# Kernel tuning notes

Measured on AMD Instinct MI355X. Metric: run time of the kernel, lower is better.

## Reference

```python
import jax, jax.numpy as jnp
import numpy as np

N, H, NIN, A, P = 256, 1024, 512, 8, 2   # agents, hid_size, num_inputs, dim_actions, comm_passes
E = N * (N - 1)                          # directed complete graph (itertools.permutations order)
_src = np.repeat(np.arange(N), N - 1)
_dst = np.concatenate([np.concatenate([np.arange(i), np.arange(i + 1, N)]) for i in range(N)])


def setup_inputs() -> dict:
    key = jax.random.key(0)
    ks = jax.random.split(key, 30)
    rn = lambda k, sh, s=0.05: (jax.random.normal(k, sh, dtype=jnp.float32) * s)
    u = jax.random.uniform(ks[0], (P, 2, E, 2), jnp.float32, 1e-6, 1.0 - 1e-6)
    gumbel = -jnp.log(-jnp.log(u))
    inp = dict(
        x=jax.random.normal(ks[1], (N, NIN), jnp.float32),
        gumbel=gumbel,
        W_enc=rn(ks[2], (NIN, H)), b_enc=jnp.zeros((H,), jnp.float32),
        ha1_W1=rn(ks[3], (2 * H, H // 2)), ha1_b1=jnp.zeros((H // 2,), jnp.float32),
        ha1_W2=rn(ks[4], (H // 2, 2)), ha1_b2=jnp.zeros((2,), jnp.float32),
        ha2_W1=rn(ks[5], (2 * H, H // 2)), ha2_b1=jnp.zeros((H // 2,), jnp.float32),
        ha2_W2=rn(ks[6], (H // 2, 2)), ha2_b2=jnp.zeros((2,), jnp.float32),
        g1_W=rn(ks[7], (H, H)), g1_b=jnp.zeros((H,), jnp.float32),
        g2_W=rn(ks[8], (H, H)), g2_b=jnp.zeros((H,), jnp.float32),
        Wf=rn(ks[9], (P, H, H)), bf=jnp.zeros((P, H), jnp.float32),
        Wc=rn(ks[10], (P, H, H)), bc=jnp.zeros((P, H), jnp.float32),
        Wv=rn(ks[11], (H, 1)), bv=jnp.zeros((1,), jnp.float32),
        Wa=rn(ks[12], (H, A)), ba=jnp.zeros((A,), jnp.float32),
        log_std=jnp.zeros((1, A), jnp.float32),
    )
    return inp


def _edge_weights(h, W1, b1, W2, b2, g, src, dst):
    # concat(h[src], h[dst]) @ W1 == h[src] @ W1[:H] + h[dst] @ W1[H:]  (avoids [E,2H] concat)
    ps = h @ W1[:H]
    pd = h @ W1[H:]
    hid = jax.nn.relu(ps[src] + pd[dst] + b1)        # [E, H/2]
    logits = hid @ W2 + b2                            # [E, 2]
    y_soft = jax.nn.softmax(logits + g, axis=-1)      # gumbel-softmax, tau=1
    y_hard = jax.nn.one_hot(jnp.argmax(y_soft, axis=-1), 2, dtype=y_soft.dtype)
    y = y_hard + y_soft - jax.lax.stop_gradient(y_soft)  # straight-through hard
    return y[:, 1]                                    # edge selected iff class 1


def _gcn(h, w, Wg, bg, src, dst):
    # PyG GCNConv(normalize=False, add_self_loops=True): out_t = sum_{s->t} Wx_s + Wx_t + b
    Wx = h @ Wg                                       # [N, H]
    Adj = jnp.zeros((N, N), h.dtype).at[dst, src].set(w)  # Adj[t, s] = edge weight s->t
    return Adj @ Wx + Wx + bg


def reference(x, gumbel, W_enc, b_enc, ha1_W1, ha1_b1, ha1_W2, ha1_b2,
              ha2_W1, ha2_b1, ha2_W2, ha2_b2, g1_W, g1_b, g2_W, g2_b,
              Wf, bf, Wc, bc, Wv, bv, Wa, ba, log_std):
    src = jnp.asarray(_src)
    dst = jnp.asarray(_dst)
    x_enc = jnp.tanh(x @ W_enc + b_enc)               # non-recurrent encoder
    hidden = x_enc
    mask = jnp.ones((N, 1), x.dtype)                  # all agents alive
    for i in range(P):
        comm = hidden * mask
        w1 = _edge_weights(hidden, ha1_W1, ha1_b1, ha1_W2, ha1_b2, gumbel[i, 0], src, dst)
        comm = _gcn(comm, w1, g1_W, g1_b, src, dst)
        w2 = _edge_weights(comm, ha2_W1, ha2_b1, ha2_W2, ha2_b2, gumbel[i, 1], src, dst)
        comm = _gcn(comm, w2, g2_W, g2_b, src, dst)
        comm = comm * mask
        c = comm @ Wc[i] + bc[i]
        hidden = jnp.tanh(x_enc + (hidden @ Wf[i] + bf[i]) + c)
    value = hidden @ Wv + bv                          # [N, 1]
    h3 = hidden.reshape(1, N, H)
    a_mean = h3 @ Wa + ba                             # [1, N, A]
    a_log_std = jnp.broadcast_to(log_std, a_mean.shape)
    return a_mean, a_log_std, jnp.exp(a_log_std), value
```

## Files before the change

### kernel.cpp

```cpp
#include <hip/hip_runtime.h>

#define N_AG 256
#define HDIM 1024
#define NINP 512
#define EDG  65280

__device__ __forceinline__ int swz8(int b, int nw) {
  return (b & 7) * (nw >> 3) + (b >> 3);
}

__device__ __forceinline__ void gcore8(const float* __restrict__ Ap, const float* __restrict__ Bp,
                                       int kIters, int ldb, float acc[8]) {
  #pragma unroll 8
  for (int k=0; k<kIters; ++k) {
    float av = Ap[(size_t)k*N_AG];
    float4 b0 = *reinterpret_cast<const float4*>(Bp + (size_t)k*ldb);
    float4 b1 = *reinterpret_cast<const float4*>(Bp + (size_t)k*ldb + 4);
    acc[0]=fmaf(av,b0.x,acc[0]); acc[1]=fmaf(av,b0.y,acc[1]);
    acc[2]=fmaf(av,b0.z,acc[2]); acc[3]=fmaf(av,b0.w,acc[3]);
    acc[4]=fmaf(av,b1.x,acc[4]); acc[5]=fmaf(av,b1.y,acc[5]);
    acc[6]=fmaf(av,b1.z,acc[6]); acc[7]=fmaf(av,b1.w,acc[7]);
  }
}

__device__ __forceinline__ float kred8(const float acc[8], int lane, int wv, int tid) {
  __shared__ float red[8][64][9];
  #pragma unroll
  for (int j=0;j<8;++j) red[wv][lane][j] = acc[j];
  __syncthreads();
  int m = tid & 63, j = tid >> 6;
  float v = 0.f;
  #pragma unroll
  for (int w=0;w<8;++w) v += red[w][m][j];
  return v;
}

__global__ __launch_bounds__(512) void prep_k(const float* w2a, const float* b2a,
                                              const float* w2b, const float* b2b,
                                              float* wd1, float* wd2, float* bd) {
  int z = blockIdx.x;
  const float* W2 = z ? w2b : w2a;
  float* wd = z ? wd2 : wd1;
  int t = threadIdx.x;
  if (t < 512) wd[t] = W2[2*t+1] - W2[2*t];
  if (t == 0) { const float* b2 = z ? b2b : b2a; bd[z] = b2[1] - b2[0]; }
}

__global__ __launch_bounds__(256) void transpose_k(const float* __restrict__ x, float* __restrict__ xT) {
  __shared__ float tile[32][33];
  int tx = threadIdx.x, ty = threadIdx.y;
  int k0 = blockIdx.x*32, m0 = blockIdx.y*32;
  #pragma unroll
  for (int i=0;i<4;++i) tile[ty*4+i][tx] = x[(size_t)(m0+ty*4+i)*NINP + k0+tx];
  __syncthreads();
  #pragma unroll
  for (int i=0;i<4;++i) xT[(size_t)(k0+ty*4+i)*N_AG + m0+tx] = tile[tx][ty*4+i];
}

__global__ __launch_bounds__(512) void enc_k(const float* __restrict__ xT, const float* __restrict__ W,
                                             const float* __restrict__ b, float* __restrict__ xeT,
                                             float* __restrict__ hA) {
  int tid = threadIdx.x, lane = tid & 63;
  int wv = __builtin_amdgcn_readfirstlane(tid >> 6);
  int id = swz8(blockIdx.x, 512);
  int mb = id & 3, n0 = (id >> 2) * 8;
  int m  = mb*64 + lane;
  float acc[8] = {0,0,0,0,0,0,0,0};
  gcore8(xT + (size_t)(wv*64)*N_AG + m, W + (size_t)(wv*64)*HDIM + n0, 64, HDIM, acc);
  float v = kred8(acc, lane, wv, tid);
  int mo = mb*64 + (tid & 63);
  int n  = n0 + (tid >> 6);
  float t0 = tanhf(v + b[n]);
  xeT[(size_t)n*N_AG + mo] = t0;
  hA [(size_t)n*N_AG + mo] = t0;
}

__global__ __launch_bounds__(512) void fused_k(const float* __restrict__ hT,
    const float* __restrict__ W1a, const float* __restrict__ W1b, const float* __restrict__ b1,
    const float* __restrict__ gW, float* __restrict__ psT, float* __restrict__ pdT,
    float* __restrict__ Wx) {
  int tid = threadIdx.x, lane = tid & 63;
  int wv = __builtin_amdgcn_readfirstlane(tid >> 6);
  int id = swz8(blockIdx.x, 1024);
  int mb = id & 3, by = id >> 2;
  const float* B; int ldb, n0, mode;
  if (by < 64)       { B = W1a; ldb = 512;  n0 = by*8;       mode = 0; }
  else if (by < 128) { B = W1b; ldb = 512;  n0 = (by-64)*8;  mode = 1; }
  else               { B = gW;  ldb = HDIM; n0 = (by-128)*8; mode = 2; }
  int m = mb*64 + lane;
  float acc[8] = {0,0,0,0,0,0,0,0};
  gcore8(hT + (size_t)(wv*128)*N_AG + m, B + (size_t)(wv*128)*ldb + n0, 128, ldb, acc);
  float v = kred8(acc, lane, wv, tid);
  int mo = mb*64 + (tid & 63);
  int n  = n0 + (tid >> 6);
  if (mode == 0)      psT[(size_t)n*N_AG + mo] = v + b1[n];
  else if (mode == 1) pdT[(size_t)n*N_AG + mo] = v;
  else                Wx [(size_t)mo*HDIM + n] = v;
}

__global__ __launch_bounds__(256) void edge2_k(const float* __restrict__ psT,
    const float* __restrict__ pdT, const float* __restrict__ wd,
    const float* __restrict__ bdp, const float* __restrict__ g, float* __restrict__ AdjT) {
  __shared__ float red[4][65];
  int tid = threadIdx.x, lane = tid & 63;
  int wv = __builtin_amdgcn_readfirstlane(tid >> 6);
  int d  = blockIdx.x*64 + lane;
  int s  = blockIdx.y;
  const float* __restrict__ ps = psT + (size_t)(wv*128)*N_AG + s;
  const float* __restrict__ wp = wd + wv*128;
  const float* __restrict__ pp = pdT + (size_t)(wv*128)*N_AG + d;
  float acc = 0.f;
  #pragma unroll 8
  for (int k=0;k<128;++k)
    acc = fmaf(fmaxf(ps[(size_t)k*N_AG] + pp[(size_t)k*N_AG], 0.f), wp[k], acc);
  red[wv][lane] = acc;
  __syncthreads();
  if (wv == 0) {
    float tot = red[0][lane] + red[1][lane] + red[2][lane] + red[3][lane];
    int e = (d==s) ? 0 : (s*255 + d - (d>s ? 1 : 0));
    float g0 = g[2*e], g1 = g[2*e+1];
    float val = (tot + bdp[0] + g1 - g0) > 0.f ? 1.f : 0.f;
    if (d==s) val = 1.f;
    AdjT[(size_t)s*N_AG + d] = val;
  }
}

__global__ __launch_bounds__(512) void adj_k(const float* __restrict__ AdjT, const float* __restrict__ Wx,
                                             const float* __restrict__ gb, float* __restrict__ commT) {
  int tid = threadIdx.x, lane = tid & 63;
  int wv = __builtin_amdgcn_readfirstlane(tid >> 6);
  int id = swz8(blockIdx.x, 512);
  int mb = id & 3, n0 = (id >> 2) * 8;
  int m  = mb*64 + lane;
  float acc[8] = {0,0,0,0,0,0,0,0};
  gcore8(AdjT + (size_t)(wv*32)*N_AG + m, Wx + (size_t)(wv*32)*HDIM + n0, 32, HDIM, acc);
  float v = kred8(acc, lane, wv, tid);
  int mo = mb*64 + (tid & 63);
  int n  = n0 + (tid >> 6);
  commT[(size_t)n*N_AG + mo] = v + gb[n];
}

__global__ __launch_bounds__(512) void combine2_k(const float* __restrict__ hT, const float* __restrict__ cT,
    const float* __restrict__ Wf, const float* __restrict__ Wc, const float* __restrict__ xeT,
    const float* __restrict__ bfp, const float* __restrict__ bcp, float* __restrict__ hOut) {
  int tid = threadIdx.x, lane = tid & 63;
  int wv = __builtin_amdgcn_readfirstlane(tid >> 6);
  int id = swz8(blockIdx.x, 512);
  int mb = id & 3, n0 = (id >> 2) * 8;
  int m  = mb*64 + lane;
  int sel = wv >> 2, kb = (wv & 3)*256;
  const float* A = (sel ? cT : hT) + (size_t)kb*N_AG + m;
  const float* B = (sel ? Wc : Wf) + (size_t)kb*HDIM + n0;
  float acc[8] = {0,0,0,0,0,0,0,0};
  gcore8(A, B, 256, HDIM, acc);
  float v = kred8(acc, lane, wv, tid);
  int mo = mb*64 + (tid & 63);
  int n  = n0 + (tid >> 6);
  float r = v + xeT[(size_t)n*N_AG + mo] + bfp[n] + bcp[n];
  hOut[(size_t)n*N_AG + mo] = tanhf(r);
}

__global__ __launch_bounds__(256) void outinit_k(float* out, const float* ba, const float* ls, const float* bvp) {
  int t = blockIdx.x*256 + threadIdx.x;
  if (t < 2048) out[t] = ba[t & 7];
  else if (t < 4096) out[t] = ls[t & 7];
  else if (t < 6144) out[t] = expf(ls[t & 7]);
  else if (t < 6400) out[t] = bvp[0];
}

__global__ __launch_bounds__(64) void outpart_k(const float* __restrict__ hT, const float* __restrict__ Wa,
                                                const float* __restrict__ Wv, float* out) {
  int m = blockIdx.x*64 + threadIdx.x;
  int c0 = blockIdx.y*64;
  float acc[8] = {0,0,0,0,0,0,0,0};
  float av = 0.f;
  for (int c=c0; c<c0+64; ++c) {
    float h = hT[(size_t)c*N_AG + m];
    const float* wa = Wa + (size_t)c*8;
    #pragma unroll
    for (int j=0;j<8;++j) acc[j] = fmaf(h, wa[j], acc[j]);
    av = fmaf(h, Wv[c], av);
  }
  #pragma unroll
  for (int j=0;j<8;++j) atomicAdd(&out[m*8+j], acc[j]);
  atomicAdd(&out[6144+m], av);
}

extern "C" void kernel_launch(void* const* d_in, const int* in_sizes, int n_in,
                              void* d_out, int out_size, void* d_ws, size_t ws_size,
                              hipStream_t stream) {
  const float* x     = (const float*)d_in[0];
  const float* gum   = (const float*)d_in[1];
  const float* W_enc = (const float*)d_in[2];
  const float* b_enc = (const float*)d_in[3];
  const float* ha1W1 = (const float*)d_in[4];
  const float* ha1b1 = (const float*)d_in[5];
  const float* ha1W2 = (const float*)d_in[6];
  const float* ha1b2 = (const float*)d_in[7];
  const float* ha2W1 = (const float*)d_in[8];
  const float* ha2b1 = (const float*)d_in[9];
  const float* ha2W2 = (const float*)d_in[10];
  const float* ha2b2 = (const float*)d_in[11];
  const float* g1W = (const float*)d_in[12];
  const float* g1b = (const float*)d_in[13];
  const float* g2W = (const float*)d_in[14];
  const float* g2b = (const float*)d_in[15];
  const float* Wf  = (const float*)d_in[16];
  const float* bfp = (const float*)d_in[17];
  const float* Wc  = (const float*)d_in[18];
  const float* bcp = (const float*)d_in[19];
  const float* Wv  = (const float*)d_in[20];
  const float* bvp = (const float*)d_in[21];
  const float* Wa  = (const float*)d_in[22];
  const float* ba  = (const float*)d_in[23];
  const float* ls  = (const float*)d_in[24];
  float* out = (float*)d_out;
  float* w = (float*)d_ws;

  float* xT    = w;
  float* xeT   = w + 131072;
  float* hA    = w + 393216;
  float* hB    = w + 655360;
  float* commT = w + 917504;
  float* psT   = w + 1179648;
  float* pdT   = w + 1310720;
  float* Wx    = w + 1441792;
  float* AdjT  = w + 1703936;
  float* wd1   = w + 1769472;
  float* wd2   = w + 1769984;
  float* bd    = w + 1770496;

  prep_k<<<dim3(2),dim3(512),0,stream>>>(ha1W2, ha1b2, ha2W2, ha2b2, wd1, wd2, bd);
  transpose_k<<<dim3(16,8),dim3(32,8),0,stream>>>(x, xT);
  enc_k<<<dim3(512),dim3(512),0,stream>>>(xT, W_enc, b_enc, xeT, hA);

  for (int i=0;i<2;++i) {
    float* hIn  = i ? hB : hA;
    float* hOut = i ? hA : hB;

    fused_k<<<dim3(1024),dim3(512),0,stream>>>(hIn, ha1W1, ha1W1 + 1024*512, ha1b1, g1W, psT, pdT, Wx);
    edge2_k<<<dim3(4,256),dim3(256),0,stream>>>(psT, pdT, wd1, bd+0, gum + (size_t)(i*2+0)*EDG*2, AdjT);
    adj_k<<<dim3(512),dim3(512),0,stream>>>(AdjT, Wx, g1b, commT);

    fused_k<<<dim3(1024),dim3(512),0,stream>>>(commT, ha2W1, ha2W1 + 1024*512, ha2b1, g2W, psT, pdT, Wx);
    edge2_k<<<dim3(4,256),dim3(256),0,stream>>>(psT, pdT, wd2, bd+1, gum + (size_t)(i*2+1)*EDG*2, AdjT);
    adj_k<<<dim3(512),dim3(512),0,stream>>>(AdjT, Wx, g2b, commT);

    combine2_k<<<dim3(512),dim3(512),0,stream>>>(hIn, commT, Wf + (size_t)i*HDIM*HDIM, Wc + (size_t)i*HDIM*HDIM,
                                                 xeT, bfp + i*HDIM, bcp + i*HDIM, hOut);
  }

  outinit_k<<<dim3(25),dim3(256),0,stream>>>(out, ba, ls, bvp);
  outpart_k<<<dim3(4,16),dim3(64),0,stream>>>(hA, Wa, Wv, out);
}
```

Baseline: 382.6 us.

## Software-pipeline GEMM inner loop, template leading dimension, merge prep kernels

Rewrites the shared GEMM inner loop to prefetch the next two k-rows of A and B into registers while computing the current two, with the B leading dimension as a compile-time template parameter. This aims to hide global load latency and simplify address arithmetic. It also adds occupancy hints to launch bounds and merges the W2-difference prep kernel with the transpose kernel to save one launch. The price is higher register pressure from the double-buffered operands, which the occupancy hint may push toward spilling.

```diff
diff --git a/kernel.cpp b/kernel.cpp
--- a/kernel.cpp
+++ b/kernel.cpp
@@ -9,18 +9,35 @@
   return (b & 7) * (nw >> 3) + (b >> 3);
 }
 
+#define FMA8(av, B0, B1) \
+  acc[0]=fmaf(av,B0.x,acc[0]); acc[1]=fmaf(av,B0.y,acc[1]); \
+  acc[2]=fmaf(av,B0.z,acc[2]); acc[3]=fmaf(av,B0.w,acc[3]); \
+  acc[4]=fmaf(av,B1.x,acc[4]); acc[5]=fmaf(av,B1.y,acc[5]); \
+  acc[6]=fmaf(av,B1.z,acc[6]); acc[7]=fmaf(av,B1.w,acc[7]);
+
+template<int LDB>
 __device__ __forceinline__ void gcore8(const float* __restrict__ Ap, const float* __restrict__ Bp,
-                                       int kIters, int ldb, float acc[8]) {
-  #pragma unroll 8
-  for (int k=0; k<kIters; ++k) {
-    float av = Ap[(size_t)k*N_AG];
-    float4 b0 = *reinterpret_cast<const float4*>(Bp + (size_t)k*ldb);
-    float4 b1 = *reinterpret_cast<const float4*>(Bp + (size_t)k*ldb + 4);
-    acc[0]=fmaf(av,b0.x,acc[0]); acc[1]=fmaf(av,b0.y,acc[1]);
-    acc[2]=fmaf(av,b0.z,acc[2]); acc[3]=fmaf(av,b0.w,acc[3]);
-    acc[4]=fmaf(av,b1.x,acc[4]); acc[5]=fmaf(av,b1.y,acc[5]);
-    acc[6]=fmaf(av,b1.z,acc[6]); acc[7]=fmaf(av,b1.w,acc[7]);
-  }
+                                       int kIters, float acc[8]) {
+  float a0 = Ap[0];
+  float a1 = Ap[N_AG];
+  float4 p0 = *reinterpret_cast<const float4*>(Bp);
+  float4 p1 = *reinterpret_cast<const float4*>(Bp + 4);
+  float4 q0 = *reinterpret_cast<const float4*>(Bp + LDB);
+  float4 q1 = *reinterpret_cast<const float4*>(Bp + LDB + 4);
+  #pragma unroll 2
+  for (int k = 0; k < kIters - 2; k += 2) {
+    float na0 = Ap[(size_t)(k+2)*N_AG];
+    float na1 = Ap[(size_t)(k+3)*N_AG];
+    float4 np0 = *reinterpret_cast<const float4*>(Bp + (size_t)(k+2)*LDB);
+    float4 np1 = *reinterpret_cast<const float4*>(Bp + (size_t)(k+2)*LDB + 4);
+    float4 nq0 = *reinterpret_cast<const float4*>(Bp + (size_t)(k+3)*LDB);
+    float4 nq1 = *reinterpret_cast<const float4*>(Bp + (size_t)(k+3)*LDB + 4);
+    FMA8(a0, p0, p1);
+    FMA8(a1, q0, q1);
+    a0 = na0; a1 = na1; p0 = np0; p1 = np1; q0 = nq0; q1 = nq1;
+  }
+  FMA8(a0, p0, p1);
+  FMA8(a1, q0, q1);
 }
 
 __device__ __forceinline__ float kred8(const float acc[8], int lane, int wv, int tid) {
@@ -35,21 +52,24 @@
   return v;
 }
 
-__global__ __launch_bounds__(512) void prep_k(const float* w2a, const float* b2a,
-                                              const float* w2b, const float* b2b,
-                                              float* wd1, float* wd2, float* bd) {
-  int z = blockIdx.x;
-  const float* W2 = z ? w2b : w2a;
-  float* wd = z ? wd2 : wd1;
-  int t = threadIdx.x;
-  if (t < 512) wd[t] = W2[2*t+1] - W2[2*t];
-  if (t == 0) { const float* b2 = z ? b2b : b2a; bd[z] = b2[1] - b2[0]; }
-}
-
-__global__ __launch_bounds__(256) void transpose_k(const float* __restrict__ x, float* __restrict__ xT) {
+__global__ __launch_bounds__(256) void prepT_k(const float* __restrict__ x, float* __restrict__ xT,
+                                               const float* w2a, const float* b2a,
+                                               const float* w2b, const float* b2b,
+                                               float* wd1, float* wd2, float* bd) {
+  int bid = blockIdx.x;
+  if (bid >= 128) {
+    int z = bid - 128;
+    const float* W2 = z ? w2b : w2a;
+    float* wd = z ? wd2 : wd1;
+    int t = threadIdx.x;
+    wd[t]       = W2[2*t+1]       - W2[2*t];
+    wd[t+256]   = W2[2*(t+256)+1] - W2[2*(t+256)];
+    if (t == 0) { const float* b2 = z ? b2b : b2a; bd[z] = b2[1] - b2[0]; }
+    return;
+  }
   __shared__ float tile[32][33];
-  int tx = threadIdx.x, ty = threadIdx.y;
-  int k0 = blockIdx.x*32, m0 = blockIdx.y*32;
+  int tx = threadIdx.x & 31, ty = threadIdx.x >> 5;
+  int k0 = (bid & 15)*32, m0 = (bid >> 4)*32;
   #pragma unroll
   for (int i=0;i<4;++i) tile[ty*4+i][tx] = x[(size_t)(m0+ty*4+i)*NINP + k0+tx];
   __syncthreads();
@@ -57,16 +77,16 @@
   for (int i=0;i<4;++i) xT[(size_t)(k0+ty*4+i)*N_AG + m0+tx] = tile[tx][ty*4+i];
 }
 
-__global__ __launch_bounds__(512) void enc_k(const float* __restrict__ xT, const float* __restrict__ W,
-                                             const float* __restrict__ b, float* __restrict__ xeT,
-                                             float* __restrict__ hA) {
+__global__ __launch_bounds__(512, 8) void enc_k(const float* __restrict__ xT, const float* __restrict__ W,
+                                                const float* __restrict__ b, float* __restrict__ xeT,
+                                                float* __restrict__ hA) {
   int tid = threadIdx.x, lane = tid & 63;
   int wv = __builtin_amdgcn_readfirstlane(tid >> 6);
   int id = swz8(blockIdx.x, 512);
   int mb = id & 3, n0 = (id >> 2) * 8;
   int m  = mb*64 + lane;
   float acc[8] = {0,0,0,0,0,0,0,0};
-  gcore8(xT + (size_t)(wv*64)*N_AG + m, W + (size_t)(wv*64)*HDIM + n0, 64, HDIM, acc);
+  gcore8<HDIM>(xT + (size_t)(wv*64)*N_AG + m, W + (size_t)(wv*64)*HDIM + n0, 64, acc);
   float v = kred8(acc, lane, wv, tid);
   int mo = mb*64 + (tid & 63);
   int n  = n0 + (tid >> 6);
@@ -75,7 +95,7 @@
   hA [(size_t)n*N_AG + mo] = t0;
 }
 
-__global__ __launch_bounds__(512) void fused_k(const float* __restrict__ hT,
+__global__ __launch_bounds__(512, 8) void fused_k(const float* __restrict__ hT,
     const float* __restrict__ W1a, const float* __restrict__ W1b, const float* __restrict__ b1,
     const float* __restrict__ gW, float* __restrict__ psT, float* __restrict__ pdT,
     float* __restrict__ Wx) {
@@ -83,13 +103,19 @@
   int wv = __builtin_amdgcn_readfirstlane(tid >> 6);
   int id = swz8(blockIdx.x, 1024);
   int mb = id & 3, by = id >> 2;
-  const float* B; int ldb, n0, mode;
-  if (by < 64)       { B = W1a; ldb = 512;  n0 = by*8;       mode = 0; }
-  else if (by < 128) { B = W1b; ldb = 512;  n0 = (by-64)*8;  mode = 1; }
-  else               { B = gW;  ldb = HDIM; n0 = (by-128)*8; mode = 2; }
   int m = mb*64 + lane;
   float acc[8] = {0,0,0,0,0,0,0,0};
-  gcore8(hT + (size_t)(wv*128)*N_AG + m, B + (size_t)(wv*128)*ldb + n0, 128, ldb, acc);
+  int n0, mode;
+  if (by < 64) {
+    n0 = by*8; mode = 0;
+    gcore8<512>(hT + (size_t)(wv*128)*N_AG + m, W1a + (size_t)(wv*128)*512 + n0, 128, acc);
+  } else if (by < 128) {
+    n0 = (by-64)*8; mode = 1;
+    gcore8<512>(hT + (size_t)(wv*128)*N_AG + m, W1b + (size_t)(wv*128)*512 + n0, 128, acc);
+  } else {
+    n0 = (by-128)*8; mode = 2;
+    gcore8<HDIM>(hT + (size_t)(wv*128)*N_AG + m, gW + (size_t)(wv*128)*HDIM + n0, 128, acc);
+  }
   float v = kred8(acc, lane, wv, tid);
   int mo = mb*64 + (tid & 63);
   int n  = n0 + (tid >> 6);
@@ -125,22 +151,22 @@
   }
 }
 
-__global__ __launch_bounds__(512) void adj_k(const float* __restrict__ AdjT, const float* __restrict__ Wx,
-                                             const float* __restrict__ gb, float* __restrict__ commT) {
+__global__ __launch_bounds__(512, 8) void adj_k(const float* __restrict__ AdjT, const float* __restrict__ Wx,
+                                                const float* __restrict__ gb, float* __restrict__ commT) {
   int tid = threadIdx.x, lane = tid & 63;
   int wv = __builtin_amdgcn_readfirstlane(tid >> 6);
   int id = swz8(blockIdx.x, 512);
   int mb = id & 3, n0 = (id >> 2) * 8;
   int m  = mb*64 + lane;
   float acc[8] = {0,0,0,0,0,0,0,0};
-  gcore8(AdjT + (size_t)(wv*32)*N_AG + m, Wx + (size_t)(wv*32)*HDIM + n0, 32, HDIM, acc);
+  gcore8<HDIM>(AdjT + (size_t)(wv*32)*N_AG + m, Wx + (size_t)(wv*32)*HDIM + n0, 32, acc);
   float v = kred8(acc, lane, wv, tid);
   int mo = mb*64 + (tid & 63);
   int n  = n0 + (tid >> 6);
   commT[(size_t)n*N_AG + mo] = v + gb[n];
 }
 
-__global__ __launch_bounds__(512) void combine2_k(const float* __restrict__ hT, const float* __restrict__ cT,
+__global__ __launch_bounds__(512, 8) void combine2_k(const float* __restrict__ hT, const float* __restrict__ cT,
     const float* __restrict__ Wf, const float* __restrict__ Wc, const float* __restrict__ xeT,
     const float* __restrict__ bfp, const float* __restrict__ bcp, float* __restrict__ hOut) {
   int tid = threadIdx.x, lane = tid & 63;
@@ -152,7 +178,7 @@
   const float* A = (sel ? cT : hT) + (size_t)kb*N_AG + m;
   const float* B = (sel ? Wc : Wf) + (size_t)kb*HDIM + n0;
   float acc[8] = {0,0,0,0,0,0,0,0};
-  gcore8(A, B, 256, HDIM, acc);
+  gcore8<HDIM>(A, B, 256, acc);
   float v = kred8(acc, lane, wv, tid);
   int mo = mb*64 + (tid & 63);
   int n  = n0 + (tid >> 6);
@@ -230,8 +256,7 @@
   float* wd2   = w + 1769984;
   float* bd    = w + 1770496;
 
-  prep_k<<<dim3(2),dim3(512),0,stream>>>(ha1W2, ha1b2, ha2W2, ha2b2, wd1, wd2, bd);
-  transpose_k<<<dim3(16,8),dim3(32,8),0,stream>>>(x, xT);
+  prepT_k<<<dim3(130),dim3(256),0,stream>>>(x, xT, ha1W2, ha1b2, ha2W2, ha2b2, wd1, wd2, bd);
   enc_k<<<dim3(512),dim3(512),0,stream>>>(xT, W_enc, b_enc, xeT, hA);
 
   for (int i=0;i<2;++i) {
```

New measurement: 365.1 us. 4.6% less time.
